# Performance work log

Hardware: AMD Instinct MI355X
Metric: run time of the kernel (lower is better)

Reference implementation:

```python
import jax, jax.numpy as jnp
import numpy as np

NUM_HEADS = 12
KEEP_RATE = 0.7


def setup_inputs() -> dict:
    key = jax.random.key(0)
    ks = jax.random.split(key, 5)
    B, N, C = 64, 197, 768
    x = jax.random.normal(ks[0], (B, N, C), dtype=jnp.float32)
    qkv_w = jax.random.normal(ks[1], (3 * C, C), dtype=jnp.float32) * (C ** -0.5)
    qkv_b = jax.random.normal(ks[2], (3 * C,), dtype=jnp.float32) * 0.02
    proj_w = jax.random.normal(ks[3], (C, C), dtype=jnp.float32) * (C ** -0.5)
    proj_b = jax.random.normal(ks[4], (C,), dtype=jnp.float32) * 0.02
    return {"x": x, "qkv_w": qkv_w, "qkv_b": qkv_b, "proj_w": proj_w, "proj_b": proj_b}


def reference(x, qkv_w, qkv_b, proj_w, proj_b):
    B, N, C = x.shape
    H = NUM_HEADS
    D = C // H
    scale = D ** -0.5
    # qkv projection: [B,N,3C] -> [3,B,H,N,D]
    qkv = (x @ qkv_w.T + qkv_b).reshape(B, N, 3, H, D).transpose(2, 0, 3, 1, 4)
    q, k, v = qkv[0], qkv[1], qkv[2]
    # full materialized attention (required for cls-row extraction)
    attn = jax.nn.softmax(jnp.einsum('bhqd,bhkd->bhqk', q, k) * scale, axis=-1)
    out = jnp.einsum('bhqk,bhkd->bqhd', attn, v).reshape(B, N, C)
    out = out @ proj_w.T + proj_b
    # EViT token pruning: cls-token attention over non-cls keys, head-averaged
    left_tokens = int(KEEP_RATE * (N - 1))  # 137
    cls_attn = attn[:, :, 0, 1:].mean(axis=1)  # [B, N-1]
    _, idx = jax.lax.top_k(cls_attn, left_tokens)  # sorted descending, like torch.topk
    index = jnp.broadcast_to(idx[:, :, None], (B, left_tokens, C))
    return (out, index, idx, cls_attn)
```

## Files before the change

kernel.cpp:

```cpp
#include <hip/hip_runtime.h>
#include <hip/hip_bf16.h>
#include <stdint.h>

constexpr int BATCH = 64;
constexpr int NTOK  = 197;
constexpr int CDIM  = 768;
constexpr int NH    = 12;
constexpr int HD    = 64;
constexpr int MROWS = BATCH * NTOK;
constexpr int MPAD  = 12800;
constexpr int NROWT = MPAD / 128;
constexpr int LEFT  = 137;
constexpr int KPAD  = 224;
constexpr int BH    = BATCH * NH;
constexpr int SPAD  = 208;

constexpr size_t OUT_OFF_OUT   = 0;
constexpr size_t OUT_OFF_INDEX = (size_t)BATCH * NTOK * CDIM;
constexpr size_t OUT_OFF_IDX   = OUT_OFF_INDEX + (size_t)BATCH * LEFT * CDIM;
constexpr size_t OUT_OFF_CLS   = OUT_OFF_IDX + (size_t)BATCH * LEFT;

constexpr size_t WS_CLSPH = 0;
constexpr size_t WS_CLSF  = WS_CLSPH + (size_t)BH * (NTOK - 1);
constexpr size_t WS_IDXI  = WS_CLSF  + (size_t)BATCH * (NTOK - 1);
constexpr size_t WS_Q0    = WS_IDXI  + (size_t)BATCH * LEFT;
constexpr size_t WS_XB    = WS_Q0  + (size_t)BATCH * CDIM;
constexpr size_t WS_WB    = WS_XB  + (size_t)MPAD * CDIM / 2;
constexpr size_t WS_PB    = WS_WB  + (size_t)3 * CDIM * CDIM / 2;
constexpr size_t WS_QB    = WS_PB  + (size_t)CDIM * CDIM / 2;
constexpr size_t WS_KB    = WS_QB  + (size_t)BH * NTOK * HD / 2;
constexpr size_t WS_VTB   = WS_KB  + (size_t)BH * NTOK * HD / 2;
constexpr size_t WS_AOB   = WS_VTB + (size_t)BH * HD * KPAD / 2;
constexpr size_t WS_U     = WS_AOB + (size_t)MPAD * CDIM / 2;
constexpr size_t WS_S     = WS_U   + (size_t)BH * CDIM;

typedef __attribute__((ext_vector_type(8))) short short8;
typedef __attribute__((ext_vector_type(4))) float floatx4;

__device__ __forceinline__ ushort f2bf(float x) {
    __hip_bfloat16 h = __float2bfloat16(x);
    return *(ushort*)&h;
}

__device__ __forceinline__ void load_lds16(const ushort* g, ushort* l) {
    __builtin_amdgcn_global_load_lds(
        (const __attribute__((address_space(1))) uint32_t*)(uintptr_t)g,
        (__attribute__((address_space(3))) uint32_t*)(uint32_t)(uintptr_t)l,
        16, 0, 0);
}

constexpr int X_N4  = MROWS * CDIM / 4;
constexpr int X_NP4 = MPAD * CDIM / 4;
constexpr int W_N4  = 3 * CDIM * CDIM / 4;
constexpr int P_N4  = CDIM * CDIM / 4;
constexpr int CAST_TOTAL = X_NP4 + W_N4 + P_N4;

__global__ __launch_bounds__(256) void cast_all_kernel(const float* __restrict__ x,
                                                       const float* __restrict__ qkv_w,
                                                       const float* __restrict__ proj_w,
                                                       ushort* __restrict__ xb,
                                                       ushort* __restrict__ wb,
                                                       ushort* __restrict__ pb) {
    int i = blockIdx.x * 256 + threadIdx.x;
    const float* src;
    ushort* dst;
    int j, valid;
    if (i < X_NP4) {
        src = x; dst = xb; j = i; valid = (j < X_N4);
    } else if (i < X_NP4 + W_N4) {
        src = qkv_w; dst = wb; j = i - X_NP4; valid = 1;
    } else if (i < CAST_TOTAL) {
        src = proj_w; dst = pb; j = i - X_NP4 - W_N4; valid = 1;
    } else {
        return;
    }
    ushort4 h4 = make_ushort4(0, 0, 0, 0);
    if (valid) {
        float4 a = ((const float4*)src)[j];
        h4 = make_ushort4(f2bf(a.x), f2bf(a.y), f2bf(a.z), f2bf(a.w));
    }
    ((ushort4*)dst)[j] = h4;
}

__global__ __launch_bounds__(256) void u_kernel(const float* __restrict__ x,
                                                const float* __restrict__ qkv_w,
                                                const float* __restrict__ qkv_b,
                                                float* __restrict__ U,
                                                float* __restrict__ qbW) {
    const int bh = blockIdx.x;
    const int b  = bh / NH;
    const int h  = bh - b * NH;
    const int t  = threadIdx.x;
    const int wv   = t >> 6;
    const int lane = t & 63;

    __shared__ float x0s[CDIM];
    __shared__ float q0s[HD];

    if (t < 192) ((float4*)x0s)[t] = ((const float4*)(x + (size_t)b * NTOK * CDIM))[t];
    __syncthreads();

    for (int i = 0; i < 16; ++i) {
        const int cl = wv * 16 + i;
        const int c  = h * HD + cl;
        const float* wr = qkv_w + (size_t)c * CDIM;
        float s = 0.f;
#pragma unroll
        for (int k = 0; k < 3; ++k) {
            float4 xv  = *(const float4*)(x0s + lane * 4 + k * 256);
            float4 wv4 = *(const float4*)(wr  + lane * 4 + k * 256);
            s += xv.x * wv4.x + xv.y * wv4.y + xv.z * wv4.z + xv.w * wv4.w;
        }
#pragma unroll
        for (int off = 32; off >= 1; off >>= 1) s += __shfl_xor(s, off);
        if (lane == 0) q0s[cl] = s + qkv_b[c];
    }
    __syncthreads();

    if (wv == 0) {
        float p = q0s[lane] * qkv_b[CDIM + h * HD + lane];
#pragma unroll
        for (int off = 32; off >= 1; off >>= 1) p += __shfl_xor(p, off);
        if (lane == 0) qbW[bh] = p;
    }

    const float* wk = qkv_w + (size_t)(CDIM + h * HD) * CDIM;
    float a0 = 0.f, a1 = 0.f, a2 = 0.f;
    for (int d = 0; d < HD; d++) {
        const float qd = q0s[d];
        const float* row = wk + (size_t)d * CDIM;
        a0 = fmaf(qd, row[t],       a0);
        a1 = fmaf(qd, row[t + 256], a1);
        a2 = fmaf(qd, row[t + 512], a2);
    }
    float* ub = U + (size_t)bh * CDIM;
    ub[t] = a0; ub[t + 256] = a1; ub[t + 512] = a2;
}

__global__ __launch_bounds__(256) void score_kernel(const float* __restrict__ x,
                                                    const float* __restrict__ U,
                                                    float* __restrict__ S) {
    const int wv   = threadIdx.x >> 6;
    const int lane = threadIdx.x & 63;
    const int j    = blockIdx.x * 4 + wv;
    const int b    = blockIdx.y;
    if (j >= NTOK) return;

    const float* xr = x + ((size_t)b * NTOK + j) * CDIM;
    float4 xv[3];
#pragma unroll
    for (int i = 0; i < 3; i++) xv[i] = *(const float4*)(xr + lane * 4 + i * 256);

    for (int h = 0; h < NH; h++) {
        const float* ur = U + (size_t)(b * NH + h) * CDIM;
        float s = 0.f;
#pragma unroll
        for (int i = 0; i < 3; i++) {
            float4 uv = *(const float4*)(ur + lane * 4 + i * 256);
            s += xv[i].x * uv.x + xv[i].y * uv.y + xv[i].z * uv.z + xv[i].w * uv.w;
        }
#pragma unroll
        for (int off = 32; off >= 1; off >>= 1) s += __shfl_xor(s, off);
        if (lane == 0) S[(size_t)(b * NH + h) * SPAD + j] = s;
    }
}

template <int MODE, int NCOLT>
__global__ __launch_bounds__(256, 4) void mfma_gemm128(
    const ushort* __restrict__ A, const ushort* __restrict__ W,
    const float* __restrict__ bias,
    float* __restrict__ O0f, ushort* __restrict__ O0q,
    ushort* __restrict__ O1k, ushort* __restrict__ O2vd,
    int Mvalid, int N) {
    constexpr int K   = CDIM;
    constexpr int BK  = 32;
    constexpr int NTK = K / BK;
    __shared__ ushort sA[2 * 128 * BK];
    __shared__ ushort sB[2 * 128 * BK];

    const int t    = threadIdx.x;
    const int lane = t & 63;
    const int w    = t >> 6;
    const int wm   = (w >> 1) * 64;
    const int wn   = (w & 1) * 64;
    const int fr   = lane & 15;
    const int fq   = lane >> 4;
    const int f3   = lane & 3;

    int row, col;
    {
        constexpr int nwg = NROWT * NCOLT;
        constexpr int q = nwg >> 3, r = nwg & 7;
        const int xcd = blockIdx.x & 7, lin = blockIdx.x >> 3;
        const int wg = (xcd < r ? xcd * (q + 1) : r * (q + 1) + (xcd - r) * q) + lin;
        row = wg / NCOLT; col = wg - row * NCOLT;
    }
    const int rowBase = row * 128;
    const int colBase = col * 128;

    auto stage = [&](const ushort* __restrict__ G, ushort* dst, int grow0, int kt) {
#pragma unroll
        for (int i = 0; i < 2; ++i) {
            const int l  = i * 256 + t;
            const int rl = l >> 2;
            const int sl = (l & 3) ^ (rl & 3);
            load_lds16(G + (size_t)(grow0 + rl) * K + kt * BK + sl * 8,
                       dst + l * 8);
        }
    };

    floatx4 acc[4][4];
#pragma unroll
    for (int i = 0; i < 4; ++i)
#pragma unroll
        for (int j = 0; j < 4; ++j)
#pragma unroll
            for (int r2 = 0; r2 < 4; ++r2) acc[i][j][r2] = 0.f;

    const int s0 = (fq ^ f3) * 8;

    stage(A, sA, rowBase, 0);
    stage(W, sB, colBase, 0);

    for (int kt = 0; kt < NTK; ++kt) {
        __syncthreads();
        const int cb = (kt & 1) << 12;
        if (kt + 1 < NTK) {
            stage(A, sA + (cb ^ 4096), rowBase, kt + 1);
            stage(W, sB + (cb ^ 4096), colBase, kt + 1);
        }

        const ushort* pa = sA + cb + (wm + fr) * BK;
        const ushort* pb = sB + cb + (wn + fr) * BK;
        short8 af[4], bf[4];
#pragma unroll
        for (int i = 0; i < 4; ++i) {
            af[i] = *(const short8*)(pa + i * 512 + s0);
            bf[i] = *(const short8*)(pb + i * 512 + s0);
        }
#pragma unroll
        for (int i = 0; i < 4; ++i)
#pragma unroll
            for (int j = 0; j < 4; ++j)
                acc[i][j] = __builtin_amdgcn_mfma_f32_16x16x32_bf16(
                    af[i], bf[j], acc[i][j], 0, 0, 0);
    }

#pragma unroll
    for (int j = 0; j < 4; ++j) {
        const int nn = colBase + wn + j * 16 + fr;
        const float bq = bias[nn];
        if (MODE == 0) {
#pragma unroll
            for (int i = 0; i < 4; ++i) {
                const int mb = rowBase + wm + i * 16 + fq * 4;
#pragma unroll
                for (int r2 = 0; r2 < 4; ++r2) {
                    const int mm = mb + r2;
                    if (mm < Mvalid) O0f[(size_t)mm * N + nn] = acc[i][j][r2] + bq;
                }
            }
        } else {
            const int which = nn / CDIM;
            const int nc    = nn - which * CDIM;
            const int h     = nc >> 6;
            const int d     = nc & 63;
#pragma unroll
            for (int i = 0; i < 4; ++i) {
                const int mb = rowBase + wm + i * 16 + fq * 4;
#pragma unroll
                for (int r2 = 0; r2 < 4; ++r2) {
                    const int mm = mb + r2;
                    if (mm < Mvalid) {
                        const int b   = mm / NTOK;
                        const int tok = mm - b * NTOK;
                        const int bh  = b * NH + h;
                        const ushort val = f2bf(acc[i][j][r2] + bq);
                        if (which == 0)      O0q[((size_t)bh * NTOK + tok) * HD + d] = val;
                        else if (which == 1) O1k[((size_t)bh * NTOK + tok) * HD + d] = val;
                        else                 O2vd[(size_t)mm * CDIM + nc] = val;
                    }
                }
            }
        }
    }
}

__global__ __launch_bounds__(256) void attn_mfma_kernel(const ushort* __restrict__ Qb,
                                                        const ushort* __restrict__ Kb,
                                                        const ushort* __restrict__ Vd,
                                                        ushort* __restrict__ AOb) {
    const int bh = blockIdx.x;
    const int b  = bh / NH;
    const int h  = bh - b * NH;
    const int t  = threadIdx.x;
    const int wv   = t >> 6;
    const int lane = t & 63;
    const int qc   = lane & 15;
    const int quad = lane >> 4;

    constexpr int VSTR = KPAD + 8;
    __shared__ ushort Vt[HD][VSTR];
    __shared__ ushort Pl[4][4][16][32];
    __shared__ float  alf[4][4][16], lf[4][4][16];

    {
        const int d  = t & 63;
        const int tt = t >> 6;
        const ushort* src = Vd + (size_t)b * NTOK * CDIM + h * HD + d;
        for (int tok0 = 0; tok0 < KPAD; tok0 += 4) {
            const int tok = tok0 + tt;
            ushort v = 0;
            if (tok < NTOK) v = src[(size_t)tok * CDIM];
            Vt[d][tok] = v;
        }
    }

    const ushort* Qh = Qb + (size_t)bh * NTOK * HD;
    const ushort* Kh = Kb + (size_t)bh * NTOK * HD;

    const int tile0 = (wv == 0) ? 0 : 4 + (wv - 1) * 3;
    const int ntv   = (wv == 0) ? 4 : 3;

    short8 qf[4][2];
#pragma unroll
    for (int ti = 0; ti < 4; ++ti) {
        if (ti < ntv) {
            const int qrow = min((tile0 + ti) * 16 + qc, NTOK - 1);
            qf[ti][0] = *(const short8*)(Qh + (size_t)qrow * HD + quad * 8);
            qf[ti][1] = *(const short8*)(Qh + (size_t)qrow * HD + 32 + quad * 8);
        }
    }

    floatx4 o[4][4];
#pragma unroll
    for (int ti = 0; ti < 4; ++ti)
#pragma unroll
        for (int s = 0; s < 4; ++s)
#pragma unroll
            for (int r = 0; r < 4; ++r) o[ti][s][r] = 0.f;
    float m[4], l[4];
#pragma unroll
    for (int ti = 0; ti < 4; ++ti) { m[ti] = -INFINITY; l[ti] = 0.f; }

    __syncthreads();

    for (int c0 = 0; c0 < NTOK; c0 += 32) {
        const int kr0 = min(c0 + qc, NTOK - 1);
        const int kr1 = min(c0 + 16 + qc, NTOK - 1);
        const short8 kf00 = *(const short8*)(Kh + (size_t)kr0 * HD + quad * 8);
        const short8 kf01 = *(const short8*)(Kh + (size_t)kr0 * HD + 32 + quad * 8);
        const short8 kf10 = *(const short8*)(Kh + (size_t)kr1 * HD + quad * 8);
        const short8 kf11 = *(const short8*)(Kh + (size_t)kr1 * HD + 32 + quad * 8);

#pragma unroll
        for (int ti = 0; ti < 4; ++ti) {
            if (ti >= ntv) continue;
            floatx4 s0 = {0.f, 0.f, 0.f, 0.f}, s1 = {0.f, 0.f, 0.f, 0.f};
            s0 = __builtin_amdgcn_mfma_f32_16x16x32_bf16(kf00, qf[ti][0], s0, 0, 0, 0);
            s0 = __builtin_amdgcn_mfma_f32_16x16x32_bf16(kf01, qf[ti][1], s0, 0, 0, 0);
            s1 = __builtin_amdgcn_mfma_f32_16x16x32_bf16(kf10, qf[ti][0], s1, 0, 0, 0);
            s1 = __builtin_amdgcn_mfma_f32_16x16x32_bf16(kf11, qf[ti][1], s1, 0, 0, 0);

            float sv[8];
            float mloc = -INFINITY;
#pragma unroll
            for (int r = 0; r < 4; ++r) {
                const int key0 = c0 + quad * 4 + r;
                const int key1 = key0 + 16;
                sv[r]     = (key0 < NTOK) ? s0[r] * 0.125f : -1e30f;
                sv[4 + r] = (key1 < NTOK) ? s1[r] * 0.125f : -1e30f;
                mloc = fmaxf(mloc, fmaxf(sv[r], sv[4 + r]));
            }
            mloc = fmaxf(mloc, __shfl_xor(mloc, 16));
            mloc = fmaxf(mloc, __shfl_xor(mloc, 32));
            const float mnew  = fmaxf(m[ti], mloc);
            const float alpha = __expf(m[ti] - mnew);
            float p[8], ps = 0.f;
#pragma unroll
            for (int i = 0; i < 8; ++i) { p[i] = __expf(sv[i] - mnew); ps += p[i]; }
            ps += __shfl_xor(ps, 16);
            ps += __shfl_xor(ps, 32);
            l[ti] = l[ti] * alpha + ps;
            m[ti] = mnew;

#pragma unroll
            for (int r = 0; r < 4; ++r) {
                Pl[wv][ti][qc][quad * 4 + r]      = f2bf(p[r]);
                Pl[wv][ti][qc][16 + quad * 4 + r] = f2bf(p[4 + r]);
            }
            if (quad == 0) alf[wv][ti][qc] = alpha;
        }
        __syncthreads();

        short8 pf[4];
#pragma unroll
        for (int ti = 0; ti < 4; ++ti) {
            if (ti >= ntv) continue;
            pf[ti] = *(const short8*)&Pl[wv][ti][qc][quad * 8];
            float ar[4];
#pragma unroll
            for (int r = 0; r < 4; ++r) ar[r] = alf[wv][ti][quad * 4 + r];
#pragma unroll
            for (int s = 0; s < 4; ++s)
#pragma unroll
                for (int r = 0; r < 4; ++r) o[ti][s][r] *= ar[r];
        }

#pragma unroll
        for (int s = 0; s < 4; ++s) {
            const short8 vf = *(const short8*)&Vt[s * 16 + qc][c0 + quad * 8];
#pragma unroll
            for (int ti = 0; ti < 4; ++ti)
                if (ti < ntv)
                    o[ti][s] = __builtin_amdgcn_mfma_f32_16x16x32_bf16(
                        pf[ti], vf, o[ti][s], 0, 0, 0);
        }
        __syncthreads();
    }

#pragma unroll
    for (int ti = 0; ti < 4; ++ti)
        if (ti < ntv && quad == 0) lf[wv][ti][qc] = l[ti];
    __syncthreads();

#pragma unroll
    for (int ti = 0; ti < 4; ++ti) {
        if (ti >= ntv) continue;
        const int qt = tile0 + ti;
#pragma unroll
        for (int r = 0; r < 4; ++r) {
            const int tok = qt * 16 + quad * 4 + r;
            if (tok >= NTOK) continue;
            const float inv = 1.f / lf[wv][ti][quad * 4 + r];
            ushort* dst = AOb + ((size_t)(b * NTOK + tok)) * CDIM + h * HD;
#pragma unroll
            for (int s = 0; s < 4; ++s) dst[s * 16 + qc] = f2bf(o[ti][s][r] * inv);
        }
    }
}

__global__ __launch_bounds__(256) void topk_fused_kernel(const float* __restrict__ S,
                                                         const float* __restrict__ qbW,
                                                         int* __restrict__ idxI,
                                                         float* __restrict__ idxOut,
                                                         float* __restrict__ outCls) {
    const int b    = blockIdx.x;
    const int t    = threadIdx.x;
    const int lane = t & 63;
    const int w    = t >> 6;

    __shared__ float qbv[NH];
    __shared__ float redm[4], reds[4];
    __shared__ float vsh[NTOK - 1];

    if (t < NH) qbv[t] = qbW[b * NH + t];
    __syncthreads();

    float macc = 0.f;
    for (int h = 0; h < NH; ++h) {
        const float qb = qbv[h];
        const float sv = (t < NTOK) ? (S[(size_t)(b * NH + h) * SPAD + t] + qb) * 0.125f
                                    : -INFINITY;
        float mloc = sv;
#pragma unroll
        for (int off = 32; off >= 1; off >>= 1) mloc = fmaxf(mloc, __shfl_xor(mloc, off));
        if (lane == 0) redm[w] = mloc;
        __syncthreads();
        const float mx = fmaxf(fmaxf(redm[0], redm[1]), fmaxf(redm[2], redm[3]));
        const float p = (t < NTOK) ? expf(sv - mx) : 0.f;
        float ls = p;
#pragma unroll
        for (int off = 32; off >= 1; off >>= 1) ls += __shfl_xor(ls, off);
        if (lane == 0) reds[w] = ls;
        __syncthreads();
        const float denom = (reds[0] + reds[1]) + (reds[2] + reds[3]);
        macc += p / denom;
        __syncthreads();
    }

    if (t >= 1 && t < NTOK) {
        const float val = macc * (1.f / 12.f);
        vsh[t - 1] = val;
        outCls[(size_t)b * (NTOK - 1) + (t - 1)] = val;
    }
    __syncthreads();

    if (t < NTOK - 1) {
        const float vi = vsh[t];
        int rank = 0;
        for (int j = 0; j < NTOK - 1; j++) {
            const float vj = vsh[j];
            rank += (vj > vi) || (vj == vi && j < t);
        }
        if (rank < LEFT) {
            idxI[b * LEFT + rank]   = t;
            idxOut[b * LEFT + rank] = (float)t;
        }
    }
}

__global__ void fill_index_kernel(const int* __restrict__ idxI,
                                  float* __restrict__ dst) {
    int tid = blockIdx.x * 256 + threadIdx.x;
    constexpr int C4 = CDIM / 4;
    if (tid >= BATCH * LEFT * C4) return;
    float v = (float)idxI[tid / C4];
    ((float4*)dst)[tid] = make_float4(v, v, v, v);
}

extern "C" void kernel_launch(void* const* d_in, const int* in_sizes, int n_in,
                              void* d_out, int out_size, void* d_ws, size_t ws_size,
                              hipStream_t stream) {
    const float* x      = (const float*)d_in[0];
    const float* qkv_w  = (const float*)d_in[1];
    const float* qkv_b  = (const float*)d_in[2];
    const float* proj_w = (const float*)d_in[3];
    const float* proj_b = (const float*)d_in[4];
    float* out = (float*)d_out;

    float*  ws    = (float*)d_ws;
    int*    idxi  = (int*)(ws + WS_IDXI);
    float*  qbW   = ws + WS_Q0;
    ushort* xb    = (ushort*)(ws + WS_XB);
    ushort* wb    = (ushort*)(ws + WS_WB);
    ushort* pb    = (ushort*)(ws + WS_PB);
    ushort* qb    = (ushort*)(ws + WS_QB);
    ushort* kb    = (ushort*)(ws + WS_KB);
    ushort* vd    = (ushort*)(ws + WS_VTB);
    ushort* aob   = (ushort*)(ws + WS_AOB);
    float*  U     = ws + WS_U;
    float*  S     = ws + WS_S;

    cast_all_kernel<<<CAST_TOTAL / 256, 256, 0, stream>>>(x, qkv_w, proj_w, xb, wb, pb);

    u_kernel<<<BH, 256, 0, stream>>>(x, qkv_w, qkv_b, U, qbW);
    score_kernel<<<dim3((NTOK + 3) / 4, BATCH), 256, 0, stream>>>(x, U, S);

    mfma_gemm128<1, 18><<<NROWT * 18, 256, 0, stream>>>(
        xb, wb, qkv_b, nullptr, qb, kb, vd, MROWS, 3 * CDIM);

    attn_mfma_kernel<<<BH, 256, 0, stream>>>(qb, kb, vd, aob);

    mfma_gemm128<0, 6><<<NROWT * 6, 256, 0, stream>>>(
        aob, pb, proj_b, out + OUT_OFF_OUT, nullptr, nullptr, nullptr,
        MROWS, CDIM);

    topk_fused_kernel<<<BATCH, 256, 0, stream>>>(S, qbW, idxi,
                                                 out + OUT_OFF_IDX,
                                                 out + OUT_OFF_CLS);

    fill_index_kernel<<<((size_t)BATCH * LEFT * (CDIM / 4) + 255) / 256, 256, 0, stream>>>(
        idxi, out + OUT_OFF_INDEX);
}
```

Measured before the change: 326.9 us.

## Fuse prep kernels, hide index fill in QKV GEMM, vectorize V transpose

Merges the bf16 cast kernel and the U/q0 kernel into a single prep launch. The top-k stage now runs before the QKV GEMM, so the index-broadcast fill rides along as extra blocks of that GEMM launch. Score blocks now stage each batch's U rows in shared memory with 8 waves per block. The attention kernel's V transpose now uses 16-byte vector loads instead of scalar strided loads. Together these aim to cut launch count and serialized small kernels and to improve memory efficiency, at the cost of extra blocks inside the GEMM launch and more LDS bank conflicts on the transpose writes.

```diff
diff --git a/kernel.cpp b/kernel.cpp
--- a/kernel.cpp
+++ b/kernel.cpp
@@ -54,43 +54,38 @@
 constexpr int W_N4  = 3 * CDIM * CDIM / 4;
 constexpr int P_N4  = CDIM * CDIM / 4;
 constexpr int CAST_TOTAL = X_NP4 + W_N4 + P_N4;
-
-__global__ __launch_bounds__(256) void cast_all_kernel(const float* __restrict__ x,
-                                                       const float* __restrict__ qkv_w,
-                                                       const float* __restrict__ proj_w,
-                                                       ushort* __restrict__ xb,
-                                                       ushort* __restrict__ wb,
-                                                       ushort* __restrict__ pb) {
-    int i = blockIdx.x * 256 + threadIdx.x;
-    const float* src;
-    ushort* dst;
-    int j, valid;
-    if (i < X_NP4) {
-        src = x; dst = xb; j = i; valid = (j < X_N4);
-    } else if (i < X_NP4 + W_N4) {
-        src = qkv_w; dst = wb; j = i - X_NP4; valid = 1;
-    } else if (i < CAST_TOTAL) {
-        src = proj_w; dst = pb; j = i - X_NP4 - W_N4; valid = 1;
-    } else {
+constexpr int CASTB = CAST_TOTAL / 256;
+
+__global__ __launch_bounds__(256) void prep_kernel(const float* __restrict__ x,
+                                                   const float* __restrict__ qkv_w,
+                                                   const float* __restrict__ proj_w,
+                                                   const float* __restrict__ qkv_b,
+                                                   ushort* __restrict__ xb,
+                                                   ushort* __restrict__ wb,
+                                                   ushort* __restrict__ pb,
+                                                   float* __restrict__ U,
+                                                   float* __restrict__ qbW) {
+    const int bk = blockIdx.x;
+    const int t  = threadIdx.x;
+
+    if (bk < CASTB) {
+        const int i = bk * 256 + t;
+        const float* src; ushort* dst; int j, valid;
+        if (i < X_NP4)             { src = x;      dst = xb; j = i;                valid = (j < X_N4); }
+        else if (i < X_NP4 + W_N4) { src = qkv_w;  dst = wb; j = i - X_NP4;        valid = 1; }
+        else                       { src = proj_w; dst = pb; j = i - X_NP4 - W_N4; valid = 1; }
+        ushort4 h4 = make_ushort4(0, 0, 0, 0);
+        if (valid) {
+            float4 a = ((const float4*)src)[j];
+            h4 = make_ushort4(f2bf(a.x), f2bf(a.y), f2bf(a.z), f2bf(a.w));
+        }
+        ((ushort4*)dst)[j] = h4;
         return;
     }
-    ushort4 h4 = make_ushort4(0, 0, 0, 0);
-    if (valid) {
-        float4 a = ((const float4*)src)[j];
-        h4 = make_ushort4(f2bf(a.x), f2bf(a.y), f2bf(a.z), f2bf(a.w));
-    }
-    ((ushort4*)dst)[j] = h4;
-}
-
-__global__ __launch_bounds__(256) void u_kernel(const float* __restrict__ x,
-                                                const float* __restrict__ qkv_w,
-                                                const float* __restrict__ qkv_b,
-                                                float* __restrict__ U,
-                                                float* __restrict__ qbW) {
-    const int bh = blockIdx.x;
+
+    const int bh = bk - CASTB;
     const int b  = bh / NH;
     const int h  = bh - b * NH;
-    const int t  = threadIdx.x;
     const int wv   = t >> 6;
     const int lane = t & 63;
 
@@ -137,13 +132,19 @@
     ub[t] = a0; ub[t + 256] = a1; ub[t + 512] = a2;
 }
 
-__global__ __launch_bounds__(256) void score_kernel(const float* __restrict__ x,
+__global__ __launch_bounds__(512) void score_kernel(const float* __restrict__ x,
                                                     const float* __restrict__ U,
                                                     float* __restrict__ S) {
+    const int b    = blockIdx.y;
     const int wv   = threadIdx.x >> 6;
     const int lane = threadIdx.x & 63;
-    const int j    = blockIdx.x * 4 + wv;
-    const int b    = blockIdx.y;
+
+    __shared__ float Us[NH][CDIM];
+    for (int i = threadIdx.x; i < NH * (CDIM / 4); i += 512)
+        ((float4*)Us)[i] = ((const float4*)(U + (size_t)b * NH * CDIM))[i];
+    __syncthreads();
+
+    const int j = blockIdx.x * 8 + wv;
     if (j >= NTOK) return;
 
     const float* xr = x + ((size_t)b * NTOK + j) * CDIM;
@@ -152,7 +153,7 @@
     for (int i = 0; i < 3; i++) xv[i] = *(const float4*)(xr + lane * 4 + i * 256);
 
     for (int h = 0; h < NH; h++) {
-        const float* ur = U + (size_t)(b * NH + h) * CDIM;
+        const float* ur = Us[h];
         float s = 0.f;
 #pragma unroll
         for (int i = 0; i < 3; i++) {
@@ -165,18 +166,32 @@
     }
 }
 
-template <int MODE, int NCOLT>
+constexpr int FILLB    = 256;
+constexpr int FILL_TOT = BATCH * LEFT * (CDIM / 4);
+
+template <int MODE, int NCOLT, bool DOFILL>
 __global__ __launch_bounds__(256, 4) void mfma_gemm128(
     const ushort* __restrict__ A, const ushort* __restrict__ W,
     const float* __restrict__ bias,
     float* __restrict__ O0f, ushort* __restrict__ O0q,
     ushort* __restrict__ O1k, ushort* __restrict__ O2vd,
+    const int* __restrict__ idxI, float* __restrict__ fillDst,
     int Mvalid, int N) {
     constexpr int K   = CDIM;
     constexpr int BK  = 32;
     constexpr int NTK = K / BK;
+    constexpr int nwg = NROWT * NCOLT;
     __shared__ ushort sA[2 * 128 * BK];
     __shared__ ushort sB[2 * 128 * BK];
+
+    if (DOFILL && blockIdx.x >= nwg) {
+        const int fb = blockIdx.x - nwg;
+        for (int i = fb * 256 + (int)threadIdx.x; i < FILL_TOT; i += FILLB * 256) {
+            const float v = (float)idxI[i / (CDIM / 4)];
+            ((float4*)fillDst)[i] = make_float4(v, v, v, v);
+        }
+        return;
+    }
 
     const int t    = threadIdx.x;
     const int lane = t & 63;
@@ -189,7 +204,6 @@
 
     int row, col;
     {
-        constexpr int nwg = NROWT * NCOLT;
         constexpr int q = nwg >> 3, r = nwg & 7;
         const int xcd = blockIdx.x & 7, lin = blockIdx.x >> 3;
         const int wg = (xcd < r ? xcd * (q + 1) : r * (q + 1) + (xcd - r) * q) + lin;
@@ -305,14 +319,18 @@
     __shared__ float  alf[4][4][16], lf[4][4][16];
 
     {
-        const int d  = t & 63;
-        const int tt = t >> 6;
-        const ushort* src = Vd + (size_t)b * NTOK * CDIM + h * HD + d;
-        for (int tok0 = 0; tok0 < KPAD; tok0 += 4) {
-            const int tok = tok0 + tt;
-            ushort v = 0;
-            if (tok < NTOK) v = src[(size_t)tok * CDIM];
-            Vt[d][tok] = v;
+        for (int idx = t; idx < NTOK * 8; idx += 256) {
+            const int tok = idx >> 3;
+            const int d0  = (idx & 7) * 8;
+            const short8 v = *(const short8*)(
+                Vd + ((size_t)(b * NTOK + tok)) * CDIM + h * HD + d0);
+#pragma unroll
+            for (int jj = 0; jj < 8; ++jj) Vt[d0 + jj][tok] = (ushort)v[jj];
+        }
+        for (int idx = t; idx < (KPAD - NTOK) * HD; idx += 256) {
+            const int tok = NTOK + (idx >> 6);
+            const int d   = idx & 63;
+            Vt[d][tok] = 0;
         }
     }
 
@@ -500,15 +518,6 @@
     }
 }
 
-__global__ void fill_index_kernel(const int* __restrict__ idxI,
-                                  float* __restrict__ dst) {
-    int tid = blockIdx.x * 256 + threadIdx.x;
-    constexpr int C4 = CDIM / 4;
-    if (tid >= BATCH * LEFT * C4) return;
-    float v = (float)idxI[tid / C4];
-    ((float4*)dst)[tid] = make_float4(v, v, v, v);
-}
-
 extern "C" void kernel_launch(void* const* d_in, const int* in_sizes, int n_in,
                               void* d_out, int out_size, void* d_ws, size_t ws_size,
                               hipStream_t stream) {
@@ -532,24 +541,22 @@
     float*  U     = ws + WS_U;
     float*  S     = ws + WS_S;
 
-    cast_all_kernel<<<CAST_TOTAL / 256, 256, 0, stream>>>(x, qkv_w, proj_w, xb, wb, pb);
-
-    u_kernel<<<BH, 256, 0, stream>>>(x, qkv_w, qkv_b, U, qbW);
-    score_kernel<<<dim3((NTOK + 3) / 4, BATCH), 256, 0, stream>>>(x, U, S);
-
-    mfma_gemm128<1, 18><<<NROWT * 18, 256, 0, stream>>>(
-        xb, wb, qkv_b, nullptr, qb, kb, vd, MROWS, 3 * CDIM);
-
-    attn_mfma_kernel<<<BH, 256, 0, stream>>>(qb, kb, vd, aob);
-
-    mfma_gemm128<0, 6><<<NROWT * 6, 256, 0, stream>>>(
-        aob, pb, proj_b, out + OUT_OFF_OUT, nullptr, nullptr, nullptr,
-        MROWS, CDIM);
+    prep_kernel<<<CASTB + BH, 256, 0, stream>>>(x, qkv_w, proj_w, qkv_b,
+                                                xb, wb, pb, U, qbW);
+
+    score_kernel<<<dim3((NTOK + 7) / 8, BATCH), 512, 0, stream>>>(x, U, S);
 
     topk_fused_kernel<<<BATCH, 256, 0, stream>>>(S, qbW, idxi,
                                                  out + OUT_OFF_IDX,
                                                  out + OUT_OFF_CLS);
 
-    fill_index_kernel<<<((size_t)BATCH * LEFT * (CDIM / 4) + 255) / 256, 256, 0, stream>>>(
-        idxi, out + OUT_OFF_INDEX);
-}
+    mfma_gemm128<1, 18, true><<<NROWT * 18 + FILLB, 256, 0, stream>>>(
+        xb, wb, qkv_b, nullptr, qb, kb, vd,
+        idxi, out + OUT_OFF_INDEX, MROWS, 3 * CDIM);
+
+    attn_mfma_kernel<<<BH, 256, 0, stream>>>(qb, kb, vd, aob);
+
+    mfma_gemm128<0, 6, false><<<NROWT * 6, 256, 0, stream>>>(
+        aob, pb, proj_b, out + OUT_OFF_OUT, nullptr, nullptr, nullptr,
+        nullptr, nullptr, MROWS, CDIM);
+}
```

After: 330.5 us. No clear change (+1.1%).
